# Kernel optimization log

Measured on AMD Instinct MI355X. Metric: run time of the kernel, lower is better.

## Reference

```python
import jax, jax.numpy as jnp
import numpy as np

NUM_HEADS = 32
ROPE_BASE = 10000.0


def _rope_tables(seq_len, dim):
    inv_freq = 1.0 / (ROPE_BASE ** (jnp.arange(0, dim, 2, dtype=jnp.float32) / dim))
    t = jnp.arange(seq_len, dtype=jnp.float32)
    freqs = jnp.outer(t, inv_freq)                      # [S, dim/2]
    emb = jnp.concatenate([freqs, freqs], axis=-1)      # [S, dim]
    return jnp.cos(emb), jnp.sin(emb)


def _rotate_half(x):
    x1, x2 = jnp.split(x, 2, axis=-1)
    return jnp.concatenate([-x2, x1], axis=-1)


def setup_inputs() -> dict:
    key = jax.random.key(0)
    ks = jax.random.split(key, 5)
    B, T, C = 1, 4096, 4096
    hidden_states = jax.random.normal(ks[0], (B, T, C), dtype=jnp.float32)
    position_ids = jnp.arange(B * T, dtype=jnp.int64 if jax.config.jax_enable_x64 else jnp.int32).reshape(B, T)
    s = 0.02
    Wq = jax.random.normal(ks[1], (C, C), dtype=jnp.float32) * s
    Wk = jax.random.normal(ks[2], (C, C), dtype=jnp.float32) * s
    Wv = jax.random.normal(ks[3], (C, C), dtype=jnp.float32) * s
    Wo = jax.random.normal(ks[4], (C, C), dtype=jnp.float32) * s
    return {"hidden_states": hidden_states, "position_ids": position_ids,
            "Wq": Wq, "Wk": Wk, "Wv": Wv, "Wo": Wo}


def reference(hidden_states, position_ids, Wq, Wk, Wv, Wo):
    B, T, C = hidden_states.shape
    nh = NUM_HEADS
    hs = C // nh

    # Projections (torch Linear: x @ W.T), split heads -> [B, nh, T, hs]
    q = (hidden_states @ Wq.T).reshape(B, T, nh, hs).transpose(0, 2, 1, 3)
    k = (hidden_states @ Wk.T).reshape(B, T, nh, hs).transpose(0, 2, 1, 3)
    v = (hidden_states @ Wv.T).reshape(B, T, nh, hs).transpose(0, 2, 1, 3)

    # RoPE (prefill: kv_len == T)
    cos, sin = _rope_tables(T, hs)                      # [T, hs]
    cos_b = cos[position_ids][:, None]                  # [B, 1, T, hs]
    sin_b = sin[position_ids][:, None]
    q = q * cos_b + _rotate_half(q) * sin_b
    k = k * cos_b + _rotate_half(k) * sin_b

    # Eager attention with full [B, nh, T, T] scores (faithful to source)
    scale = hs ** -0.5
    attn = jnp.einsum("bhqd,bhkd->bhqk", q, k) * scale
    causal = jnp.tril(jnp.ones((T, T), dtype=bool))     # diagonal = kv_len - T = 0
    attn = jnp.where(causal[None, None], attn, -jnp.inf)
    attn = jax.nn.softmax(attn, axis=-1)
    out = jnp.einsum("bhqk,bhkd->bhqd", attn, v)
    out = out.transpose(0, 2, 1, 3).reshape(B, T, C)
    return out @ Wo.T
```

## Files before the change

kernel.cpp:

```cpp
#include <hip/hip_runtime.h>

typedef __attribute__((ext_vector_type(8))) short short8;
typedef __attribute__((ext_vector_type(4))) short short4v;
typedef __attribute__((ext_vector_type(4))) float f32x4;

#define NH 32
#define HS 128
#define CDIM 4096
#define QBLK 256
#define KVBLK 64
#define NQT 16

__device__ __forceinline__ ushort f2bf(float f) {
  union { float f; unsigned u; } a; a.f = f;
  unsigned u = a.u;
  return (ushort)((u + 0x7FFFu + ((u >> 16) & 1u)) >> 16);
}
__device__ __forceinline__ float bf2f(ushort h) {
  union { unsigned u; float f; } a; a.u = ((unsigned)h) << 16;
  return a.f;
}
__device__ __forceinline__ unsigned cvtpk_bf16(float lo, float hi) {
  unsigned r;
  asm("v_cvt_pk_bf16_f32 %0, %1, %2" : "=v"(r) : "v"(lo), "v"(hi));
  return r;
}

__device__ __forceinline__ void gld16(const void* g, void* l) {
  __builtin_amdgcn_global_load_lds((const __attribute__((address_space(1))) void*)g,
                                   (__attribute__((address_space(3))) void*)l, 16, 0, 0);
}

__device__ __forceinline__ unsigned lds_off(const void* p) {
  return (unsigned)(uintptr_t)(const __attribute__((address_space(3))) void*)p;
}

template<int OFF>
__device__ __forceinline__ short4v ds_tr16(unsigned addr) {
  short4v r;
  asm volatile("ds_read_b64_tr_b16 %0, %1 offset:%c2" : "=v"(r) : "v"(addr), "i"(OFF));
  return r;
}

__global__ __launch_bounds__(256) void cast_bf16_kernel(const float* __restrict__ in,
                                                        ushort* __restrict__ out, int n4) {
  int i = blockIdx.x * 256 + threadIdx.x;
  if (i >= n4) return;
  float4 v = ((const float4*)in)[i];
  ushort4 o;
  o.x = f2bf(v.x); o.y = f2bf(v.y); o.z = f2bf(v.z); o.w = f2bf(v.w);
  ((ushort4*)out)[i] = o;
}

#define A00 0
#define A01 16384
#define A10 32768
#define A11 49152
#define B00 65536
#define B01 81920
#define B10 98304
#define B11 114688

template<typename OutT>
__global__ __launch_bounds__(512, 2) void gemm256(const ushort* __restrict__ A,
                                                  const ushort* __restrict__ B,
                                                  OutT* __restrict__ C) {
  __shared__ char sm[131072];
  const int tid = threadIdx.x;
  const int w = tid >> 6, lane = tid & 63, lhi = lane >> 4, llo = lane & 15;

  const int bid = blockIdx.x;
  const int x = (bid & 7) * 32 + (bid >> 3);
  const int mt = x >> 4, nt = x & 15;
  const size_t m0 = (size_t)mt * 256, n0 = (size_t)nt * 256;

  const char* A0p = (const char*)(A + m0 * 4096);
  const char* A1p = A0p + 1048576;
  const char* B0p = (const char*)(B + n0 * 4096);
  const char* B1p = B0p + 1048576;

  const int i0 = tid, i1 = tid + 512;
  const int ri0 = i0 >> 3, ri1 = i1 >> 3;
  const int cg0 = (i0 & 7) ^ (((ri0 >> 2) & 1) << 1);
  const int cg1 = (i1 & 7) ^ (((ri1 >> 2) & 1) << 1);
  const int off0 = ri0 * 8192 + cg0 * 16;
  const int off1 = ri1 * 8192 + cg1 * 16;
  const unsigned sd0 = (unsigned)(w * 1024);
  const unsigned sd1 = (unsigned)(8192 + w * 1024);

  const int sw = ((llo >> 2) & 1) << 1;
  const unsigned rd0 = (unsigned)((llo * 8 + ((0 * 4 + lhi) ^ sw)) * 16);
  const unsigned rd1 = (unsigned)((llo * 8 + ((1 * 4 + lhi) ^ sw)) * 16);

  const int wmg = w >> 2, wng = w & 3;
  const unsigned aE = wmg ? A01 : A00;
  const unsigned aO = wmg ? A11 : A10;
  const unsigned bE = (wng >> 1) ? B01 : B00;
  const unsigned bO = (wng >> 1) ? B11 : B10;
  const unsigned bco = (unsigned)((wng & 1) * 8192);

  f32x4 acc[8][4] = {};
  short8 a0[4], a1[4], u0[2], u1[2], v0[2], v1[2];

#define STG(PAN, K0, LB) do { \
    gld16((PAN) + (size_t)(K0) * 2 + off0, sm + (LB) + sd0); \
    gld16((PAN) + (size_t)(K0) * 2 + off1, sm + (LB) + sd1); \
  } while (0)
#define LDA(BASE, MQ) do { _Pragma("unroll") for (int m_ = 0; m_ < 4; m_++) { \
    a0[m_] = *(const short8*)(sm + (BASE) + (MQ) * 8192 + m_ * 2048 + rd0); \
    a1[m_] = *(const short8*)(sm + (BASE) + (MQ) * 8192 + m_ * 2048 + rd1); } } while (0)
#define LDB(R0, R1, BASE, NQ) do { _Pragma("unroll") for (int n_ = 0; n_ < 2; n_++) { \
    R0[n_] = *(const short8*)(sm + (BASE) + bco + (NQ) * 4096 + n_ * 2048 + rd0); \
    R1[n_] = *(const short8*)(sm + (BASE) + bco + (NQ) * 4096 + n_ * 2048 + rd1); } } while (0)
#define MM(MQ, NQ, R0, R1) do { \
    _Pragma("unroll") for (int m_ = 0; m_ < 4; m_++) _Pragma("unroll") for (int n_ = 0; n_ < 2; n_++) \
      acc[(MQ) * 4 + m_][(NQ) * 2 + n_] = __builtin_amdgcn_mfma_f32_16x16x32_bf16(a0[m_], R0[n_], acc[(MQ) * 4 + m_][(NQ) * 2 + n_], 0, 0, 0); \
    _Pragma("unroll") for (int m_ = 0; m_ < 4; m_++) _Pragma("unroll") for (int n_ = 0; n_ < 2; n_++) \
      acc[(MQ) * 4 + m_][(NQ) * 2 + n_] = __builtin_amdgcn_mfma_f32_16x16x32_bf16(a1[m_], R1[n_], acc[(MQ) * 4 + m_][(NQ) * 2 + n_], 0, 0, 0); \
  } while (0)
#define BAR1 do { __builtin_amdgcn_s_barrier(); \
    asm volatile("s_waitcnt lgkmcnt(0)" ::: "memory"); \
    __builtin_amdgcn_sched_barrier(0); \
    __builtin_amdgcn_s_setprio(1); } while (0)
#define BAR2 do { __builtin_amdgcn_s_setprio(0); __builtin_amdgcn_s_barrier(); \
    __builtin_amdgcn_sched_barrier(0); } while (0)

  STG(B0p, 0, B00); STG(B1p, 0, B01); STG(A0p, 0, A00); STG(A1p, 0, A01);
  STG(B0p, 64, B10); STG(B1p, 64, B11); STG(A0p, 64, A10); STG(A1p, 64, A11);
  asm volatile("s_waitcnt vmcnt(8)" ::: "memory");
  __builtin_amdgcn_s_barrier();
  __builtin_amdgcn_sched_barrier(0);

  for (int it = 0; it < 32; ++it) {
    const int kc = it * 128;
    const bool st = (it < 31);
    LDA(aE, 0); LDB(u0, u1, bE, 0);
    BAR1; MM(0, 0, u0, u1); BAR2;
    LDB(v0, v1, bE, 1);
    BAR1; MM(0, 1, v0, v1); BAR2;
    LDA(aE, 1);
    if (st) STG(B0p, kc + 128, B00);
    BAR1; MM(1, 1, v0, v1); BAR2;
    if (st) { STG(B1p, kc + 128, B01); STG(A0p, kc + 128, A00); }
    BAR1; MM(1, 0, u0, u1);
    __builtin_amdgcn_s_setprio(0);
    if (st) asm volatile("s_waitcnt vmcnt(6)" ::: "memory");
    else    asm volatile("s_waitcnt vmcnt(0)" ::: "memory");
    __builtin_amdgcn_s_barrier();
    __builtin_amdgcn_sched_barrier(0);
    LDA(aO, 0); LDB(u0, u1, bO, 0);
    if (st) STG(A1p, kc + 128, A01);
    BAR1; MM(0, 0, u0, u1); BAR2;
    LDB(v0, v1, bO, 1);
    BAR1; MM(0, 1, v0, v1); BAR2;
    LDA(aO, 1);
    if (st) { STG(B0p, kc + 192, B10); STG(B1p, kc + 192, B11); }
    BAR1; MM(1, 1, v0, v1); BAR2;
    if (st) { STG(A0p, kc + 192, A10); STG(A1p, kc + 192, A11); }
    BAR1; MM(1, 0, u0, u1);
    __builtin_amdgcn_s_setprio(0);
    if (st) asm volatile("s_waitcnt vmcnt(8)" ::: "memory");
    __builtin_amdgcn_s_barrier();
    __builtin_amdgcn_sched_barrier(0);
  }

  const int wm = wmg * 128, wn = wng * 64;
#pragma unroll
  for (int m = 0; m < 8; m++) {
#pragma unroll
    for (int nf = 0; nf < 4; nf++) {
      const size_t col = n0 + wn + nf * 16 + llo;
#pragma unroll
      for (int j = 0; j < 4; j++) {
        const size_t row = m0 + wm + m * 16 + lhi * 4 + j;
        if constexpr (sizeof(OutT) == 4)
          C[row * 4096 + col] = acc[m][nf][j];
        else
          C[row * 4096 + col] = f2bf(acc[m][nf][j]);
      }
    }
  }
#undef STG
#undef LDA
#undef LDB
#undef MM
#undef BAR1
#undef BAR2
}

__global__ __launch_bounds__(256) void rope_kernel(ushort* __restrict__ Q,
                                                   ushort* __restrict__ Kb,
                                                   const int* __restrict__ pos_ids,
                                                   int nrows) {
  int gid = blockIdx.x * 256 + threadIdx.x;
  int d = gid & 63;
  int row = gid >> 6;
  if (row >= nrows) return;
  int t = row >> 5;
  int pos = pos_ids[t];
  float inv = expf((float)d * -0.14391156831212788f);
  float ang = (float)pos * inv;
  float s, c;
  sincosf(ang, &s, &c);
  size_t base = (size_t)row * HS;
  {
    float x1 = bf2f(Q[base + d]), x2 = bf2f(Q[base + d + 64]);
    Q[base + d]      = f2bf(x1 * c - x2 * s);
    Q[base + d + 64] = f2bf(x2 * c + x1 * s);
  }
  {
    float x1 = bf2f(Kb[base + d]), x2 = bf2f(Kb[base + d + 64]);
    Kb[base + d]      = f2bf(x1 * c - x2 * s);
    Kb[base + d + 64] = f2bf(x2 * c + x1 * s);
  }
}

__global__ __launch_bounds__(512) void flash_attn(const ushort* __restrict__ Q,
                                                  const ushort* __restrict__ K,
                                                  const ushort* __restrict__ V,
                                                  ushort* __restrict__ O) {
  __shared__ __align__(16) ushort Ks[KVBLK * HS];
  __shared__ __align__(16) ushort Vs[KVBLK * HS];
  __shared__ __align__(16) ushort Ps[8][32 * 72];
  const int tid = threadIdx.x;
  const int w = tid >> 6, l = tid & 63, lhi = l >> 4, llo = l & 15;
  const int qbp = blockIdx.x, h = blockIdx.y;

  const int g = llo >> 2, c = llo & 3;
  const int swz = g | ((lhi & 1) << 2);
  const int c1 = c >> 1;
  const int swL = swz & 1, swH = swz & 6;
  const unsigned trbase = lds_off(Vs) + (unsigned)((lhi * 8 + g) * 256 + ((c1 ^ swL) << 4) + (c & 1) * 8);

  const int srow = tid >> 4, sch = tid & 15;
  const int schK = sch ^ (srow & 7);
  const int schV = sch ^ ((srow & 3) | (((srow >> 3) & 1) << 2));

  char* pwB = (char*)Ps[w];
  const float scale = 0.08838834764831845f;

  short8 kreg[2], vreg[2];

  for (int ph = 0; ph < 2; ph++) {
    const int qt = ph ? (NQT - 1 - qbp) : qbp;
    const int qr0 = qt * QBLK + w * 32;
    const int ntile = 4 * qt + 4;

    short8 aq[2][4];
#pragma unroll
    for (int mf = 0; mf < 2; mf++) {
      const ushort* qp = Q + (size_t)(qr0 + mf * 16 + llo) * CDIM + h * HS + lhi * 8;
#pragma unroll
      for (int ki = 0; ki < 4; ki++) aq[mf][ki] = *(const short8*)(qp + ki * 32);
    }

    f32x4 acc[2][8] = {};
    float mrow[2] = {-1e30f, -1e30f};
    float lrow[2] = {0.f, 0.f};

#pragma unroll
    for (int r = 0; r < 2; r++) {
      const size_t rb = (size_t)(srow + r * 32) * CDIM + h * HS + sch * 8;
      kreg[r] = *(const short8*)(K + rb);
      vreg[r] = *(const short8*)(V + rb);
    }
#pragma unroll
    for (int r = 0; r < 2; r++) {
      const int row = srow + r * 32;
      *(short8*)((char*)Ks + ((row * 16 + schK) << 4)) = kreg[r];
      *(short8*)((char*)Vs + ((row * 16 + schV) << 4)) = vreg[r];
    }
    __syncthreads();

    for (int t = 0; t < ntile; t++) {
      const int kv0 = t * KVBLK;
      if (t + 1 < ntile) {
        const size_t rb = (size_t)(kv0 + KVBLK + srow) * CDIM + h * HS + sch * 8;
#pragma unroll
        for (int r = 0; r < 2; r++) {
          kreg[r] = *(const short8*)(K + rb + (size_t)r * 32 * CDIM);
          vreg[r] = *(const short8*)(V + rb + (size_t)r * 32 * CDIM);
        }
      }
      const bool active = (kv0 <= qr0 + 31);
      if (active) {
        f32x4 s[2][4];
        __builtin_amdgcn_s_setprio(1);
#pragma unroll
        for (int nt = 0; nt < 4; nt++) {
          const int krow = nt * 16 + llo;
          const char* kr = (const char*)Ks + krow * 256;
          short8 kf[4];
#pragma unroll
          for (int ki = 0; ki < 4; ki++)
            kf[ki] = *(const short8*)(kr + (((ki * 4 + lhi) ^ (krow & 7)) << 4));
          f32x4 s0 = {0.f, 0.f, 0.f, 0.f}, s1 = {0.f, 0.f, 0.f, 0.f};
#pragma unroll
          for (int ki = 0; ki < 4; ki++) {
            s0 = __builtin_amdgcn_mfma_f32_16x16x32_bf16(kf[ki], aq[0][ki], s0, 0, 0, 0);
            s1 = __builtin_amdgcn_mfma_f32_16x16x32_bf16(kf[ki], aq[1][ki], s1, 0, 0, 0);
          }
          s[0][nt] = s0; s[1][nt] = s1;
        }
        __builtin_amdgcn_s_setprio(0);

        short4v vl0[8], vh0[8];
#pragma unroll
        for (int on = 0; on < 8; on++) {
          unsigned a = trbase + (unsigned)(((on * 2) ^ swH) << 4);
          vl0[on] = ds_tr16<0>(a);
          vh0[on] = ds_tr16<1024>(a);
        }

        const bool needm = (kv0 + KVBLK - 1 > qr0);
#pragma unroll
        for (int mf = 0; mf < 2; mf++) {
          const int qi = qr0 + mf * 16 + llo;
#pragma unroll
          for (int nt = 0; nt < 4; nt++) {
            const int kvb = kv0 + nt * 16 + lhi * 4;
#pragma unroll
            for (int j = 0; j < 4; j++) {
              float sv = s[mf][nt][j] * scale;
              if (needm && kvb + j > qi) sv = -1e30f;
              s[mf][nt][j] = sv;
            }
          }
        }

#pragma unroll
        for (int mf = 0; mf < 2; mf++) {
          f32x4 mm;
#pragma unroll
          for (int j = 0; j < 4; j++)
            mm[j] = fmaxf(fmaxf(s[mf][0][j], s[mf][1][j]), fmaxf(s[mf][2][j], s[mf][3][j]));
          float pmax = fmaxf(fmaxf(mm[0], mm[1]), fmaxf(mm[2], mm[3]));
          pmax = fmaxf(pmax, __shfl_xor(pmax, 16));
          pmax = fmaxf(pmax, __shfl_xor(pmax, 32));
          if (__any(pmax > mrow[mf] + 8.f)) {
            float mn = fmaxf(mrow[mf], pmax);
            float sc = __expf(mrow[mf] - mn);
            mrow[mf] = mn;
            lrow[mf] *= sc;
#pragma unroll
            for (int on = 0; on < 8; on++)
#pragma unroll
              for (int j = 0; j < 4; j++) acc[mf][on][j] *= sc;
          }
          float rs = 0.f;
#pragma unroll
          for (int nt = 0; nt < 4; nt++) {
            float p0 = __expf(s[mf][nt][0] - mrow[mf]);
            float p1 = __expf(s[mf][nt][1] - mrow[mf]);
            float p2 = __expf(s[mf][nt][2] - mrow[mf]);
            float p3 = __expf(s[mf][nt][3] - mrow[mf]);
            rs += (p0 + p1) + (p2 + p3);
            uint2 pk;
            pk.x = cvtpk_bf16(p0, p1);
            pk.y = cvtpk_bf16(p2, p3);
            *(uint2*)(pwB + (mf * 16 + llo) * 144 + nt * 32 + lhi * 8) = pk;
          }
          rs += __shfl_xor(rs, 16);
          rs += __shfl_xor(rs, 32);
          lrow[mf] += rs;
        }

        {
          short8 pf0 = *(const short8*)(pwB + llo * 144 + lhi * 16);
          short8 pf1 = *(const short8*)(pwB + (16 + llo) * 144 + lhi * 16);
          asm volatile("s_waitcnt lgkmcnt(0)" ::: "memory");
          __builtin_amdgcn_sched_barrier(0);
          __builtin_amdgcn_s_setprio(1);
#pragma unroll
          for (int on = 0; on < 8; on++) {
            short8 vf = __builtin_shufflevector(vl0[on], vh0[on], 0, 1, 2, 3, 4, 5, 6, 7);
            acc[0][on] = __builtin_amdgcn_mfma_f32_16x16x32_bf16(vf, pf0, acc[0][on], 0, 0, 0);
            acc[1][on] = __builtin_amdgcn_mfma_f32_16x16x32_bf16(vf, pf1, acc[1][on], 0, 0, 0);
          }
          __builtin_amdgcn_s_setprio(0);
        }
        {
          short8 pf0 = *(const short8*)(pwB + llo * 144 + 64 + lhi * 16);
          short8 pf1 = *(const short8*)(pwB + (16 + llo) * 144 + 64 + lhi * 16);
          short4v vl[8], vh[8];
#pragma unroll
          for (int on = 0; on < 8; on++) {
            unsigned a = trbase + (unsigned)(((on * 2) ^ swH) << 4);
            vl[on] = ds_tr16<8192>(a);
            vh[on] = ds_tr16<9216>(a);
          }
          asm volatile("s_waitcnt lgkmcnt(0)" ::: "memory");
          __builtin_amdgcn_sched_barrier(0);
          __builtin_amdgcn_s_setprio(1);
#pragma unroll
          for (int on = 0; on < 8; on++) {
            short8 vf = __builtin_shufflevector(vl[on], vh[on], 0, 1, 2, 3, 4, 5, 6, 7);
            acc[0][on] = __builtin_amdgcn_mfma_f32_16x16x32_bf16(vf, pf0, acc[0][on], 0, 0, 0);
            acc[1][on] = __builtin_amdgcn_mfma_f32_16x16x32_bf16(vf, pf1, acc[1][on], 0, 0, 0);
          }
          __builtin_amdgcn_s_setprio(0);
        }
      }

      __syncthreads();
      if (t + 1 < ntile) {
#pragma unroll
        for (int r = 0; r < 2; r++) {
          const int row = srow + r * 32;
          *(short8*)((char*)Ks + ((row * 16 + schK) << 4)) = kreg[r];
          *(short8*)((char*)Vs + ((row * 16 + schV) << 4)) = vreg[r];
        }
      }
      __syncthreads();
    }

#pragma unroll
    for (int mf = 0; mf < 2; mf++) {
      const float ri = 1.0f / lrow[mf];
      ushort* orow = O + (size_t)(qr0 + mf * 16 + llo) * CDIM + h * HS + lhi * 4;
#pragma unroll
      for (int on = 0; on < 8; on++) {
        ushort4 o4;
        o4.x = f2bf(acc[mf][on][0] * ri);
        o4.y = f2bf(acc[mf][on][1] * ri);
        o4.z = f2bf(acc[mf][on][2] * ri);
        o4.w = f2bf(acc[mf][on][3] * ri);
        *(ushort4*)(orow + on * 16) = o4;
      }
    }
  }
}

extern "C" void kernel_launch(void* const* d_in, const int* in_sizes, int n_in,
                              void* d_out, int out_size, void* d_ws, size_t ws_size,
                              hipStream_t stream) {
  const float* hs = (const float*)d_in[0];
  const int* pos = (const int*)d_in[1];
  const float* Wq = (const float*)d_in[2];
  const float* Wk = (const float*)d_in[3];
  const float* Wv = (const float*)d_in[4];
  const float* Wo = (const float*)d_in[5];
  float* out = (float*)d_out;

  const int T = 4096;
  const size_t elems = (size_t)T * CDIM;

  ushort* hsb  = (ushort*)d_ws;
  ushort* wbuf = hsb + elems;
  ushort* qb   = wbuf + elems;
  ushort* kb   = qb + elems;
  ushort* vb   = kb + elems;
  ushort* attn = hsb;

  const int n4 = (int)(elems / 4);
  const int castBlocks = (n4 + 255) / 256;

  cast_bf16_kernel<<<castBlocks, 256, 0, stream>>>(hs, hsb, n4);

  cast_bf16_kernel<<<castBlocks, 256, 0, stream>>>(Wq, wbuf, n4);
  gemm256<ushort><<<256, 512, 0, stream>>>(hsb, wbuf, qb);

  cast_bf16_kernel<<<castBlocks, 256, 0, stream>>>(Wk, wbuf, n4);
  gemm256<ushort><<<256, 512, 0, stream>>>(hsb, wbuf, kb);

  cast_bf16_kernel<<<castBlocks, 256, 0, stream>>>(Wv, wbuf, n4);
  gemm256<ushort><<<256, 512, 0, stream>>>(hsb, wbuf, vb);

  rope_kernel<<<(T * NH * 64) / 256, 256, 0, stream>>>(qb, kb, pos, T * NH);

  flash_attn<<<dim3(NQT / 2, NH), 512, 0, stream>>>(qb, kb, vb, attn);

  cast_bf16_kernel<<<castBlocks, 256, 0, stream>>>(Wo, wbuf, n4);
  gemm256<float><<<256, 512, 0, stream>>>(attn, wbuf, out);
}
```

Before: 830.0 us.

## Fuse Q/K/V projections into one 768-block GEMM launch with output-buffer scratch

Replaces three sequential 256-block GEMM launches with one 768-block grouped GEMM that picks the Q, K or V weight and output per block, so the GPU runs three full waves back to back without launch gaps or tail idling between projections. The bf16 copies of Wk and Wv are staged in the fp32 output buffer as scratch, which is safe because the final GEMM overwrites it later. It also drops the sched_barrier after several barriers, which gives the compiler more scheduling freedom but may disturb the hand-tuned interleaving.

```diff
diff --git a/kernel.cpp b/kernel.cpp
--- a/kernel.cpp
+++ b/kernel.cpp
@@ -61,46 +61,81 @@
 #define B10 98304
 #define B11 114688
 
-template<typename OutT>
-__global__ __launch_bounds__(512, 2) void gemm256(const ushort* __restrict__ A,
-                                                  const ushort* __restrict__ B,
-                                                  OutT* __restrict__ C) {
-  __shared__ char sm[131072];
-  const int tid = threadIdx.x;
-  const int w = tid >> 6, lane = tid & 63, lhi = lane >> 4, llo = lane & 15;
-
-  const int bid = blockIdx.x;
-  const int x = (bid & 7) * 32 + (bid >> 3);
-  const int mt = x >> 4, nt = x & 15;
-  const size_t m0 = (size_t)mt * 256, n0 = (size_t)nt * 256;
-
-  const char* A0p = (const char*)(A + m0 * 4096);
-  const char* A1p = A0p + 1048576;
-  const char* B0p = (const char*)(B + n0 * 4096);
-  const char* B1p = B0p + 1048576;
-
-  const int i0 = tid, i1 = tid + 512;
-  const int ri0 = i0 >> 3, ri1 = i1 >> 3;
-  const int cg0 = (i0 & 7) ^ (((ri0 >> 2) & 1) << 1);
-  const int cg1 = (i1 & 7) ^ (((ri1 >> 2) & 1) << 1);
-  const int off0 = ri0 * 8192 + cg0 * 16;
-  const int off1 = ri1 * 8192 + cg1 * 16;
-  const unsigned sd0 = (unsigned)(w * 1024);
-  const unsigned sd1 = (unsigned)(8192 + w * 1024);
-
-  const int sw = ((llo >> 2) & 1) << 1;
-  const unsigned rd0 = (unsigned)((llo * 8 + ((0 * 4 + lhi) ^ sw)) * 16);
-  const unsigned rd1 = (unsigned)((llo * 8 + ((1 * 4 + lhi) ^ sw)) * 16);
-
-  const int wmg = w >> 2, wng = w & 3;
-  const unsigned aE = wmg ? A01 : A00;
-  const unsigned aO = wmg ? A11 : A10;
-  const unsigned bE = (wng >> 1) ? B01 : B00;
-  const unsigned bO = (wng >> 1) ? B11 : B10;
-  const unsigned bco = (unsigned)((wng & 1) * 8192);
-
-  f32x4 acc[8][4] = {};
-  short8 a0[4], a1[4], u0[2], u1[2], v0[2], v1[2];
+#define GEMM_BODY(OUT_STORE)                                                       \
+  __shared__ char sm[131072];                                                      \
+  const int tid = threadIdx.x;                                                     \
+  const int w = tid >> 6, lane = tid & 63, lhi = lane >> 4, llo = lane & 15;       \
+  const char* A0p = (const char*)(A + m0 * 4096);                                  \
+  const char* A1p = A0p + 1048576;                                                 \
+  const char* B0p = (const char*)(Bp + n0 * 4096);                                 \
+  const char* B1p = B0p + 1048576;                                                 \
+  const int i0 = tid, i1 = tid + 512;                                              \
+  const int ri0 = i0 >> 3, ri1 = i1 >> 3;                                          \
+  const int cg0 = (i0 & 7) ^ (((ri0 >> 2) & 1) << 1);                              \
+  const int cg1 = (i1 & 7) ^ (((ri1 >> 2) & 1) << 1);                              \
+  const int off0 = ri0 * 8192 + cg0 * 16;                                          \
+  const int off1 = ri1 * 8192 + cg1 * 16;                                          \
+  const unsigned sd0 = (unsigned)(w * 1024);                                       \
+  const unsigned sd1 = (unsigned)(8192 + w * 1024);                                \
+  const int sw = ((llo >> 2) & 1) << 1;                                            \
+  const unsigned rd0 = (unsigned)((llo * 8 + ((0 * 4 + lhi) ^ sw)) * 16);          \
+  const unsigned rd1 = (unsigned)((llo * 8 + ((1 * 4 + lhi) ^ sw)) * 16);          \
+  const int wmg = w >> 2, wng = w & 3;                                             \
+  const unsigned aE = wmg ? A01 : A00;                                             \
+  const unsigned aO = wmg ? A11 : A10;                                             \
+  const unsigned bE = (wng >> 1) ? B01 : B00;                                      \
+  const unsigned bO = (wng >> 1) ? B11 : B10;                                      \
+  const unsigned bco = (unsigned)((wng & 1) * 8192);                               \
+  f32x4 acc[8][4] = {};                                                            \
+  short8 a0[4], a1[4], u0[2], u1[2], v0[2], v1[2];                                 \
+  STG(B0p, 0, B00); STG(B1p, 0, B01); STG(A0p, 0, A00); STG(A1p, 0, A01);          \
+  STG(B0p, 64, B10); STG(B1p, 64, B11); STG(A0p, 64, A10); STG(A1p, 64, A11);      \
+  asm volatile("s_waitcnt vmcnt(8)" ::: "memory");                                 \
+  __builtin_amdgcn_s_barrier();                                                    \
+  __builtin_amdgcn_sched_barrier(0);                                               \
+  for (int it = 0; it < 32; ++it) {                                                \
+    const int kc = it * 128;                                                       \
+    const bool st = (it < 31);                                                     \
+    LDA(aE, 0); LDB(u0, u1, bE, 0);                                                \
+    BAR1; MM(0, 0, u0, u1); BAR2;                                                  \
+    LDB(v0, v1, bE, 1);                                                            \
+    BAR1; MM(0, 1, v0, v1); BAR2;                                                  \
+    LDA(aE, 1);                                                                    \
+    if (st) STG(B0p, kc + 128, B00);                                               \
+    BAR1; MM(1, 1, v0, v1); BAR2;                                                  \
+    if (st) { STG(B1p, kc + 128, B01); STG(A0p, kc + 128, A00); }                  \
+    BAR1; MM(1, 0, u0, u1);                                                        \
+    __builtin_amdgcn_s_setprio(0);                                                 \
+    if (st) asm volatile("s_waitcnt vmcnt(6)" ::: "memory");                       \
+    else    asm volatile("s_waitcnt vmcnt(0)" ::: "memory");                       \
+    __builtin_amdgcn_s_barrier();                                                  \
+    LDA(aO, 0); LDB(u0, u1, bO, 0);                                                \
+    if (st) STG(A1p, kc + 128, A01);                                               \
+    BAR1; MM(0, 0, u0, u1); BAR2;                                                  \
+    LDB(v0, v1, bO, 1);                                                            \
+    BAR1; MM(0, 1, v0, v1); BAR2;                                                  \
+    LDA(aO, 1);                                                                    \
+    if (st) { STG(B0p, kc + 192, B10); STG(B1p, kc + 192, B11); }                  \
+    BAR1; MM(1, 1, v0, v1); BAR2;                                                  \
+    if (st) { STG(A0p, kc + 192, A10); STG(A1p, kc + 192, A11); }                  \
+    BAR1; MM(1, 0, u0, u1);                                                        \
+    __builtin_amdgcn_s_setprio(0);                                                 \
+    if (st) asm volatile("s_waitcnt vmcnt(8)" ::: "memory");                       \
+    __builtin_amdgcn_s_barrier();                                                  \
+  }                                                                                \
+  const int wm = wmg * 128, wn = wng * 64;                                         \
+  _Pragma("unroll")                                                                \
+  for (int m = 0; m < 8; m++) {                                                    \
+    _Pragma("unroll")                                                              \
+    for (int nf = 0; nf < 4; nf++) {                                               \
+      const size_t col = n0 + wn + nf * 16 + llo;                                  \
+      _Pragma("unroll")                                                            \
+      for (int j = 0; j < 4; j++) {                                                \
+        const size_t row = m0 + wm + m * 16 + lhi * 4 + j;                         \
+        OUT_STORE;                                                                 \
+      }                                                                            \
+    }                                                                              \
+  }
 
 #define STG(PAN, K0, LB) do { \
     gld16((PAN) + (size_t)(K0) * 2 + off0, sm + (LB) + sd0); \
@@ -122,71 +157,44 @@
     asm volatile("s_waitcnt lgkmcnt(0)" ::: "memory"); \
     __builtin_amdgcn_sched_barrier(0); \
     __builtin_amdgcn_s_setprio(1); } while (0)
-#define BAR2 do { __builtin_amdgcn_s_setprio(0); __builtin_amdgcn_s_barrier(); \
-    __builtin_amdgcn_sched_barrier(0); } while (0)
-
-  STG(B0p, 0, B00); STG(B1p, 0, B01); STG(A0p, 0, A00); STG(A1p, 0, A01);
-  STG(B0p, 64, B10); STG(B1p, 64, B11); STG(A0p, 64, A10); STG(A1p, 64, A11);
-  asm volatile("s_waitcnt vmcnt(8)" ::: "memory");
-  __builtin_amdgcn_s_barrier();
-  __builtin_amdgcn_sched_barrier(0);
-
-  for (int it = 0; it < 32; ++it) {
-    const int kc = it * 128;
-    const bool st = (it < 31);
-    LDA(aE, 0); LDB(u0, u1, bE, 0);
-    BAR1; MM(0, 0, u0, u1); BAR2;
-    LDB(v0, v1, bE, 1);
-    BAR1; MM(0, 1, v0, v1); BAR2;
-    LDA(aE, 1);
-    if (st) STG(B0p, kc + 128, B00);
-    BAR1; MM(1, 1, v0, v1); BAR2;
-    if (st) { STG(B1p, kc + 128, B01); STG(A0p, kc + 128, A00); }
-    BAR1; MM(1, 0, u0, u1);
-    __builtin_amdgcn_s_setprio(0);
-    if (st) asm volatile("s_waitcnt vmcnt(6)" ::: "memory");
-    else    asm volatile("s_waitcnt vmcnt(0)" ::: "memory");
-    __builtin_amdgcn_s_barrier();
-    __builtin_amdgcn_sched_barrier(0);
-    LDA(aO, 0); LDB(u0, u1, bO, 0);
-    if (st) STG(A1p, kc + 128, A01);
-    BAR1; MM(0, 0, u0, u1); BAR2;
-    LDB(v0, v1, bO, 1);
-    BAR1; MM(0, 1, v0, v1); BAR2;
-    LDA(aO, 1);
-    if (st) { STG(B0p, kc + 192, B10); STG(B1p, kc + 192, B11); }
-    BAR1; MM(1, 1, v0, v1); BAR2;
-    if (st) { STG(A0p, kc + 192, A10); STG(A1p, kc + 192, A11); }
-    BAR1; MM(1, 0, u0, u1);
-    __builtin_amdgcn_s_setprio(0);
-    if (st) asm volatile("s_waitcnt vmcnt(8)" ::: "memory");
-    __builtin_amdgcn_s_barrier();
-    __builtin_amdgcn_sched_barrier(0);
-  }
-
-  const int wm = wmg * 128, wn = wng * 64;
-#pragma unroll
-  for (int m = 0; m < 8; m++) {
-#pragma unroll
-    for (int nf = 0; nf < 4; nf++) {
-      const size_t col = n0 + wn + nf * 16 + llo;
-#pragma unroll
-      for (int j = 0; j < 4; j++) {
-        const size_t row = m0 + wm + m * 16 + lhi * 4 + j;
-        if constexpr (sizeof(OutT) == 4)
-          C[row * 4096 + col] = acc[m][nf][j];
-        else
-          C[row * 4096 + col] = f2bf(acc[m][nf][j]);
-      }
-    }
-  }
+#define BAR2 do { __builtin_amdgcn_s_setprio(0); __builtin_amdgcn_s_barrier(); } while (0)
+
+__global__ __launch_bounds__(512, 2) void gemm_qkv(const ushort* __restrict__ A,
+                                                   const ushort* __restrict__ Bq,
+                                                   const ushort* __restrict__ Bk,
+                                                   const ushort* __restrict__ Bv,
+                                                   ushort* __restrict__ Cq,
+                                                   ushort* __restrict__ Ck,
+                                                   ushort* __restrict__ Cv) {
+  const int bid = blockIdx.x;
+  const int x = (bid & 7) * 96 + (bid >> 3);
+  const int mt = x / 48, ntg = x % 48;
+  const ushort* Bp;
+  ushort* Cp;
+  int ntl;
+  if (ntg < 16)      { Bp = Bq; Cp = Cq; ntl = ntg; }
+  else if (ntg < 32) { Bp = Bk; Cp = Ck; ntl = ntg - 16; }
+  else               { Bp = Bv; Cp = Cv; ntl = ntg - 32; }
+  const size_t m0 = (size_t)mt * 256, n0 = (size_t)ntl * 256;
+  GEMM_BODY(Cp[row * 4096 + col] = f2bf(acc[m][nf][j]));
+}
+
+__global__ __launch_bounds__(512, 2) void gemm256f(const ushort* __restrict__ A,
+                                                   const ushort* __restrict__ Bp,
+                                                   float* __restrict__ C) {
+  const int bid = blockIdx.x;
+  const int x = (bid & 7) * 32 + (bid >> 3);
+  const int mt = x >> 4, nt = x & 15;
+  const size_t m0 = (size_t)mt * 256, n0 = (size_t)nt * 256;
+  GEMM_BODY(C[row * 4096 + col] = acc[m][nf][j]);
+}
+
 #undef STG
 #undef LDA
 #undef LDB
 #undef MM
 #undef BAR1
 #undef BAR2
-}
 
 __global__ __launch_bounds__(256) void rope_kernel(ushort* __restrict__ Q,
                                                    ushort* __restrict__ Kb,
@@ -450,26 +458,24 @@
   ushort* qb   = wbuf + elems;
   ushort* kb   = qb + elems;
   ushort* vb   = kb + elems;
-  ushort* attn = hsb;
+
+  ushort* wkb = (ushort*)d_out;
+  ushort* wvb = wkb + elems;
 
   const int n4 = (int)(elems / 4);
   const int castBlocks = (n4 + 255) / 256;
 
   cast_bf16_kernel<<<castBlocks, 256, 0, stream>>>(hs, hsb, n4);
-
   cast_bf16_kernel<<<castBlocks, 256, 0, stream>>>(Wq, wbuf, n4);
-  gemm256<ushort><<<256, 512, 0, stream>>>(hsb, wbuf, qb);
-
-  cast_bf16_kernel<<<castBlocks, 256, 0, stream>>>(Wk, wbuf, n4);
-  gemm256<ushort><<<256, 512, 0, stream>>>(hsb, wbuf, kb);
-
-  cast_bf16_kernel<<<castBlocks, 256, 0, stream>>>(Wv, wbuf, n4);
-  gemm256<ushort><<<256, 512, 0, stream>>>(hsb, wbuf, vb);
+  cast_bf16_kernel<<<castBlocks, 256, 0, stream>>>(Wk, wkb, n4);
+  cast_bf16_kernel<<<castBlocks, 256, 0, stream>>>(Wv, wvb, n4);
+
+  gemm_qkv<<<768, 512, 0, stream>>>(hsb, wbuf, wkb, wvb, qb, kb, vb);
 
   rope_kernel<<<(T * NH * 64) / 256, 256, 0, stream>>>(qb, kb, pos, T * NH);
 
-  flash_attn<<<dim3(NQT / 2, NH), 512, 0, stream>>>(qb, kb, vb, attn);
+  flash_attn<<<dim3(NQT / 2, NH), 512, 0, stream>>>(qb, kb, vb, hsb);
 
   cast_bf16_kernel<<<castBlocks, 256, 0, stream>>>(Wo, wbuf, n4);
-  gemm256<float><<<256, 512, 0, stream>>>(attn, wbuf, out);
-}
+  gemm256f<<<256, 512, 0, stream>>>(hsb, wbuf, out);
+}
```

New measurement: 824.0 us. No clear change (-0.7%).
